# Kernel tuning notes

Hardware: AMD Instinct MI355X
Metric: run time of the kernel (lower is better)

## Reference

```python
import jax, jax.numpy as jnp
import numpy as np

N_NODES = 100000
IN_CH, HIDDEN, OUT_CH = 128, 64, 40
N_EDGES = 1600000


def gcn_conv(x, row, col, W, b, num_nodes):
    """PyG GCNConv: x' = D^-1/2 (A+I) D^-1/2 (x W) + b, self-loops already in row/col."""
    h = x @ W  # [N, out]
    deg = jax.ops.segment_sum(jnp.ones_like(col, dtype=h.dtype), col, num_segments=num_nodes)
    dinv = jnp.where(deg > 0, jax.lax.rsqrt(deg), 0.0)  # [N]
    norm = dinv[row] * dinv[col]  # [E+N]
    msg = h[row] * norm[:, None]  # gather + scale
    out = jax.ops.segment_sum(msg, col, num_segments=num_nodes)  # scatter-add to targets
    return out + b


def setup_inputs() -> dict:
    key = jax.random.key(0)
    k = jax.random.split(key, 6)
    x = jax.random.normal(k[0], (N_NODES, IN_CH), dtype=jnp.float32)
    ei = jax.random.randint(k[1], (2, N_EDGES), 0, N_NODES, dtype=jnp.int64)
    # Glorot-style init for linear weights, zeros for biases (PyG defaults)
    W1 = jax.random.normal(k[2], (IN_CH, HIDDEN), dtype=jnp.float32) / np.sqrt(IN_CH)
    b1 = jnp.zeros((HIDDEN,), dtype=jnp.float32)
    W2 = jax.random.normal(k[3], (HIDDEN, OUT_CH), dtype=jnp.float32) / np.sqrt(HIDDEN)
    b2 = jnp.zeros((OUT_CH,), dtype=jnp.float32)
    return {"x": x, "ei": ei, "W1": W1, "b1": b1, "W2": W2, "b2": b2}


def reference(x, ei, W1, b1, W2, b2):
    num_nodes = x.shape[0]
    loop = jnp.arange(num_nodes, dtype=ei.dtype)
    row = jnp.concatenate([ei[0], loop])  # sources + self-loops
    col = jnp.concatenate([ei[1], loop])  # targets + self-loops
    h = jax.nn.relu(gcn_conv(x, row, col, W1, b1, num_nodes))
    # dropout(p=0.5) is identity in eval mode (deterministic reference)
    return gcn_conv(h, row, col, W2, b2, num_nodes)
```

## Files before the change

kernel.cpp:

```cpp
#include <hip/hip_runtime.h>
#include <hip/hip_bf16.h>
#include <math.h>

#define IN_CH 128
#define HID 64
#define OUT_CH 40
#define NBUCK 1024
#define NBSHIFT 10
#define CAP2 3125
#define CAPL 2560

typedef const __hip_bfloat16* bf16p;
typedef __attribute__((ext_vector_type(8))) short bf16x8;
typedef __attribute__((ext_vector_type(4))) float f32x4;
typedef __attribute__((ext_vector_type(8))) float f32x8;

__device__ __forceinline__ f32x8 cvt8(bf16x8 v) {
    f32x8 o;
    #pragma unroll
    for (int j = 0; j < 8; ++j) {
        unsigned int bits = ((unsigned int)(unsigned short)v[j]) << 16;
        o[j] = __uint_as_float(bits);
    }
    return o;
}

__device__ __forceinline__ bf16x8 pack8(f32x8 v) {
    bf16x8 o;
    #pragma unroll
    for (int j = 0; j < 8; ++j) {
        __hip_bfloat16 b = __float2bfloat16(v[j]);
        o[j] = *reinterpret_cast<short*>(&b);
    }
    return o;
}

__device__ __forceinline__ int bucket_of(int c, int N, float invNB) {
    int b = (int)((float)c * invNB);
    long long cB = (long long)c << NBSHIFT;
    while ((long long)(b + 1) * N <= cB) ++b;
    while (b > 0 && (long long)b * N > cB) --b;
    return b;
}

__global__ __launch_bounds__(256) void k_detectconv(const void* x, const void* ei,
        int* flags, const void* W1, const void* b1, const void* W2, const void* b2,
        float* wf, int* bincnt2) {
    __shared__ int s_f32, s_hi;
    if (threadIdx.x == 0) { s_f32 = 0; s_hi = 0; }
    __syncthreads();
    const __hip_bfloat16* xb = (const __hip_bfloat16*)x;
    const int* ii = (const int*)ei;
    int lf = 0, lh = 0;
    for (int i = threadIdx.x; i < 4096; i += 256) {
        float f = __bfloat162float(xb[i]);
        if (!(fabsf(f) <= 1e4f)) lf = 1;
        lh |= ii[2 * i + 1];
    }
    if (lf) atomicOr(&s_f32, 1);
    if (lh) atomicOr(&s_hi, 1);
    for (int i = threadIdx.x; i < NBUCK; i += 256) bincnt2[i] = 0;
    __syncthreads();
    const int isF32 = s_f32 ? 1 : 0;
    if (threadIdx.x == 0) {
        flags[0] = isF32;
        flags[1] = (s_hi == 0) ? 1 : 0;
        flags[2] = 0;
    }
    for (int i = threadIdx.x; i < 10856; i += 256) {
        const void* src; int off;
        if (i < 8192)       { src = W1; off = i; }
        else if (i < 8256)  { src = b1; off = i - 8192; }
        else if (i < 10816) { src = W2; off = i - 8256; }
        else                { src = b2; off = i - 10816; }
        wf[i] = isF32 ? ((const float*)src)[off]
                      : __bfloat162float(((bf16p)src)[off]);
    }
}

__global__ __launch_bounds__(512) void k_bin2(const int* ei, const int* flags,
        int* bincnt2, unsigned int* bins2, int E, int N, float invNB) {
    __shared__ int cnt[NBUCK], base[NBUCK];
    for (int i = threadIdx.x; i < NBUCK; i += 512) cnt[i] = 0;
    __syncthreads();
    const int i64 = flags[1];
    const int e0 = blockIdx.x * 4096;
    const int e1 = min(e0 + 4096, E);
    int e = e0 + threadIdx.x;
    for (; e + 3 * 512 < e1; e += 4 * 512) {
        int c0 = i64 ? ei[2 * (E + e)]        : ei[E + e];
        int c1 = i64 ? ei[2 * (E + e + 512)]  : ei[E + e + 512];
        int c2 = i64 ? ei[2 * (E + e + 1024)] : ei[E + e + 1024];
        int c3 = i64 ? ei[2 * (E + e + 1536)] : ei[E + e + 1536];
        atomicAdd(&cnt[bucket_of(c0, N, invNB)], 1);
        atomicAdd(&cnt[bucket_of(c1, N, invNB)], 1);
        atomicAdd(&cnt[bucket_of(c2, N, invNB)], 1);
        atomicAdd(&cnt[bucket_of(c3, N, invNB)], 1);
    }
    for (; e < e1; e += 512) {
        int c = i64 ? ei[2 * (E + e)] : ei[E + e];
        atomicAdd(&cnt[bucket_of(c, N, invNB)], 1);
    }
    __syncthreads();
    for (int i = threadIdx.x; i < NBUCK; i += 512) {
        int v = cnt[i];
        base[i] = v ? atomicAdd(&bincnt2[i], v) : 0;
        cnt[i] = 0;
    }
    __syncthreads();
    for (e = e0 + threadIdx.x; e < e1; e += 512) {
        int r, c;
        if (i64) { r = ei[2 * e]; c = ei[2 * (E + e)]; }
        else     { r = ei[e];     c = ei[E + e]; }
        int b = bucket_of(c, N, invNB);
        int nlo = (int)(((long long)b * N + NBUCK - 1) >> NBSHIFT);
        int slot = base[b] + atomicAdd(&cnt[b], 1);
        if (slot < CAP2)
            bins2[(size_t)b * CAP2 + slot] =
                ((unsigned int)r << 7) | (unsigned int)(c - nlo);
    }
}

__global__ __launch_bounds__(256) void k_csr(const unsigned int* bins2, const int* bincnt2,
        int* rowstart, float* dinv, int* erow, int N) {
    __shared__ unsigned int rc[CAPL];
    __shared__ int sdeg[256], lcur[256], red[256];
    const int s = blockIdx.x;
    const int tid = threadIdx.x;
    int part = 0;
    for (int j = tid; j < s; j += 256) part += min(bincnt2[j], CAPL);
    red[tid] = part;
    __syncthreads();
    for (int o = 128; o > 0; o >>= 1) {
        if (tid < o) red[tid] += red[tid + o];
        __syncthreads();
    }
    const int gb = red[0];
    const int nlo = (int)(((long long)s * N + NBUCK - 1) >> NBSHIFT);
    const int nhi = (int)(((long long)(s + 1) * N + NBUCK - 1) >> NBSHIFT);
    const int width = nhi - nlo;
    const int cnt = min(bincnt2[s], CAPL);

    for (int i = tid; i < cnt; i += 256) rc[i] = bins2[(size_t)s * CAP2 + i];
    sdeg[tid] = 0;
    __syncthreads();
    for (int i = tid; i < cnt; i += 256) {
        int j = (int)(rc[i] & 127u);
        if (j < width) atomicAdd(&sdeg[j], 1);
    }
    __syncthreads();
    int my = sdeg[tid];
    __syncthreads();
    for (int off = 1; off < 256; off <<= 1) {
        int t = (tid >= off) ? sdeg[tid - off] : 0;
        __syncthreads();
        sdeg[tid] += t;
        __syncthreads();
    }
    int excl = sdeg[tid] - my;
    lcur[tid] = excl;
    if (tid < width) {
        rowstart[nlo + tid] = gb + excl;
        dinv[nlo + tid] = rsqrtf((float)my + 1.0f);
    }
    if (s == NBUCK - 1 && tid == 0) rowstart[N] = gb + cnt;
    __syncthreads();
    for (int i = tid; i < cnt; i += 256) {
        unsigned int v = rc[i];
        int j = (int)(v & 127u);
        if (j < width) {
            int pos = atomicAdd(&lcur[j], 1);
            erow[gb + pos] = (int)(v >> 7);
        }
    }
}

__global__ __launch_bounds__(256) void k_gemm1_mfma(const void* x, const float* W1f,
        const float* dinv, __hip_bfloat16* h1s, const int* flags, int N) {
    __shared__ __align__(16) unsigned short wT[HID][IN_CH];
    for (int i = threadIdx.x; i < IN_CH * HID; i += 256) {
        int k = i >> 6, c = i & 63;
        __hip_bfloat16 b = __float2bfloat16(W1f[i]);
        wT[c][k] = *reinterpret_cast<unsigned short*>(&b);
    }
    __syncthreads();

    const int isF32 = flags[0];
    const int lane = threadIdx.x & 63;
    const int wid  = threadIdx.x >> 6;
    const int r = lane & 15;
    const int g = lane >> 4;

    bf16x8 bfr[4][4];
    #pragma unroll
    for (int nt = 0; nt < 4; ++nt)
        #pragma unroll
        for (int ks = 0; ks < 4; ++ks)
            bfr[nt][ks] = *(const bf16x8*)&wT[nt * 16 + r][ks * 32 + g * 8];

    const int tiles = (N + 15) >> 4;
    for (int t = blockIdx.x * 4 + wid; t < tiles; t += gridDim.x * 4) {
        const int row0 = t * 16;
        int arow = row0 + r; if (arow >= N) arow = N - 1;
        bf16x8 afr[4];
        if (!isF32) {
            const unsigned short* xr = (const unsigned short*)x + (size_t)arow * IN_CH;
            #pragma unroll
            for (int ks = 0; ks < 4; ++ks)
                afr[ks] = *(const bf16x8*)&xr[ks * 32 + g * 8];
        } else {
            const float* xr = (const float*)x + (size_t)arow * IN_CH;
            #pragma unroll
            for (int ks = 0; ks < 4; ++ks) {
                f32x4 a0 = *(const f32x4*)&xr[ks * 32 + g * 8];
                f32x4 a1 = *(const f32x4*)&xr[ks * 32 + g * 8 + 4];
                #pragma unroll
                for (int j = 0; j < 4; ++j) {
                    __hip_bfloat16 b0 = __float2bfloat16(a0[j]);
                    __hip_bfloat16 b1v = __float2bfloat16(a1[j]);
                    afr[ks][j]     = *reinterpret_cast<short*>(&b0);
                    afr[ks][j + 4] = *reinterpret_cast<short*>(&b1v);
                }
            }
        }
        f32x4 acc[4] = {};
        #pragma unroll
        for (int ks = 0; ks < 4; ++ks)
            #pragma unroll
            for (int nt = 0; nt < 4; ++nt)
                acc[nt] = __builtin_amdgcn_mfma_f32_16x16x32_bf16(afr[ks], bfr[nt][ks],
                                                                  acc[nt], 0, 0, 0);
        #pragma unroll
        for (int q = 0; q < 4; ++q) {
            int rr = row0 + g * 4 + q;
            if (rr < N) {
                float dv = dinv[rr];
                #pragma unroll
                for (int nt = 0; nt < 4; ++nt)
                    h1s[(size_t)rr * HID + nt * 16 + r] =
                        __float2bfloat16(acc[nt][q] * dv);
            }
        }
    }
}

__global__ __launch_bounds__(256) void k_agg1(const int* rowstart, const int* erow,
        const __hip_bfloat16* h1s, const float* dinv, const float* b1f,
        __hip_bfloat16* gs, int N) {
    const int lane = threadIdx.x & 63;
    const int sub = lane >> 3;
    const int co  = lane & 7;
    const f32x4 b1a = *(const f32x4*)&b1f[co * 8];
    const f32x4 b1b = *(const f32x4*)&b1f[co * 8 + 4];
    const int wstride = (gridDim.x * 256) >> 6;
    for (int w = (blockIdx.x * 256 + threadIdx.x) >> 6; w < N; w += wstride) {
        int s0 = __builtin_amdgcn_readfirstlane(rowstart[w]);
        int s1 = __builtin_amdgcn_readfirstlane(rowstart[w + 1]);
        float d = dinv[w];
        bf16x8 sv = *(const bf16x8*)&h1s[(size_t)w * HID + co * 8];
        f32x8 acc = {};
        int i = s0 + sub;
        for (; i + 8 < s1; i += 16) {
            int r0 = erow[i], r1 = erow[i + 8];
            f32x8 v0 = cvt8(*(const bf16x8*)&h1s[(size_t)r0 * HID + co * 8]);
            f32x8 v1 = cvt8(*(const bf16x8*)&h1s[(size_t)r1 * HID + co * 8]);
            #pragma unroll
            for (int j = 0; j < 8; ++j) acc[j] += v0[j] + v1[j];
        }
        if (i < s1) {
            int r0 = erow[i];
            f32x8 v0 = cvt8(*(const bf16x8*)&h1s[(size_t)r0 * HID + co * 8]);
            #pragma unroll
            for (int j = 0; j < 8; ++j) acc[j] += v0[j];
        }
        #pragma unroll
        for (int j = 0; j < 8; ++j) {
            acc[j] += __shfl_xor(acc[j], 8);
            acc[j] += __shfl_xor(acc[j], 16);
            acc[j] += __shfl_xor(acc[j], 32);
        }
        if (sub == 0) {
            f32x8 sf = cvt8(sv);
            f32x8 gv;
            #pragma unroll
            for (int j = 0; j < 4; ++j) {
                float ga = fmaxf(fmaf(d, sf[j] + acc[j], b1a[j]), 0.f);
                float gb = fmaxf(fmaf(d, sf[j + 4] + acc[j + 4], b1b[j]), 0.f);
                gv[j]     = ga * d;
                gv[j + 4] = gb * d;
            }
            *(bf16x8*)&gs[(size_t)w * HID + co * 8] = pack8(gv);
        }
    }
}

__global__ __launch_bounds__(256) void k_agg2s(const int* rowstart, const int* erow,
        const __hip_bfloat16* gs, const float* dinv, __hip_bfloat16* sbuf, int N) {
    const int lane = threadIdx.x & 63;
    const int sub = lane >> 3;
    const int co  = lane & 7;
    const int wstride = (gridDim.x * 256) >> 6;
    for (int w = (blockIdx.x * 256 + threadIdx.x) >> 6; w < N; w += wstride) {
        int s0 = __builtin_amdgcn_readfirstlane(rowstart[w]);
        int s1 = __builtin_amdgcn_readfirstlane(rowstart[w + 1]);
        float d = dinv[w];
        bf16x8 sv = *(const bf16x8*)&gs[(size_t)w * HID + co * 8];
        f32x8 acc = {};
        int i = s0 + sub;
        for (; i + 8 < s1; i += 16) {
            int r0 = erow[i], r1 = erow[i + 8];
            f32x8 v0 = cvt8(*(const bf16x8*)&gs[(size_t)r0 * HID + co * 8]);
            f32x8 v1 = cvt8(*(const bf16x8*)&gs[(size_t)r1 * HID + co * 8]);
            #pragma unroll
            for (int j = 0; j < 8; ++j) acc[j] += v0[j] + v1[j];
        }
        if (i < s1) {
            int r0 = erow[i];
            f32x8 v0 = cvt8(*(const bf16x8*)&gs[(size_t)r0 * HID + co * 8]);
            #pragma unroll
            for (int j = 0; j < 8; ++j) acc[j] += v0[j];
        }
        #pragma unroll
        for (int j = 0; j < 8; ++j) {
            acc[j] += __shfl_xor(acc[j], 8);
            acc[j] += __shfl_xor(acc[j], 16);
            acc[j] += __shfl_xor(acc[j], 32);
        }
        if (sub == 0) {
            f32x8 sf = cvt8(sv);
            f32x8 ov;
            #pragma unroll
            for (int j = 0; j < 8; ++j) ov[j] = d * (sf[j] + acc[j]);
            *(bf16x8*)&sbuf[(size_t)w * HID + co * 8] = pack8(ov);
        }
    }
}

__global__ __launch_bounds__(256) void k_gemm2_mfma(const __hip_bfloat16* sbuf,
        const float* W2f, const float* b2f, float* out, int N) {
    __shared__ __align__(16) unsigned short w2T[48][HID];
    for (int i = threadIdx.x; i < 48 * HID; i += 256) {
        int c = i >> 6, k = i & 63;
        float v = (c < OUT_CH) ? W2f[k * OUT_CH + c] : 0.f;
        __hip_bfloat16 b = __float2bfloat16(v);
        w2T[c][k] = *reinterpret_cast<unsigned short*>(&b);
    }
    __syncthreads();

    const int lane = threadIdx.x & 63;
    const int wid  = threadIdx.x >> 6;
    const int r = lane & 15;
    const int gq = lane >> 4;

    bf16x8 bfr[3][2];
    #pragma unroll
    for (int nt = 0; nt < 3; ++nt)
        #pragma unroll
        for (int ks = 0; ks < 2; ++ks)
            bfr[nt][ks] = *(const bf16x8*)&w2T[nt * 16 + r][ks * 32 + gq * 8];
    float b2v[3];
    #pragma unroll
    for (int nt = 0; nt < 3; ++nt)
        b2v[nt] = (nt * 16 + r < OUT_CH) ? b2f[nt * 16 + r] : 0.f;

    const int tiles = (N + 15) >> 4;
    for (int t = blockIdx.x * 4 + wid; t < tiles; t += gridDim.x * 4) {
        const int row0 = t * 16;
        int arow = row0 + r; if (arow >= N) arow = N - 1;
        const unsigned short* sr = (const unsigned short*)sbuf + (size_t)arow * HID;
        bf16x8 afr[2];
        afr[0] = *(const bf16x8*)&sr[gq * 8];
        afr[1] = *(const bf16x8*)&sr[32 + gq * 8];
        f32x4 acc[3] = {};
        #pragma unroll
        for (int ks = 0; ks < 2; ++ks)
            #pragma unroll
            for (int nt = 0; nt < 3; ++nt)
                acc[nt] = __builtin_amdgcn_mfma_f32_16x16x32_bf16(afr[ks], bfr[nt][ks],
                                                                  acc[nt], 0, 0, 0);
        #pragma unroll
        for (int nt = 0; nt < 3; ++nt) {
            int c = nt * 16 + r;
            #pragma unroll
            for (int q = 0; q < 4; ++q) {
                int rr = row0 + gq * 4 + q;
                if (rr < N && c < OUT_CH)
                    out[(size_t)rr * OUT_CH + c] = acc[nt][q] + b2v[nt];
            }
        }
    }
}

extern "C" void kernel_launch(void* const* d_in, const int* in_sizes, int n_in,
                              void* d_out, int out_size, void* d_ws, size_t ws_size,
                              hipStream_t stream) {
    const void* x  = d_in[0];
    const void* ei = d_in[1];
    const void* W1 = d_in[2];
    const void* b1 = d_in[3];
    const void* W2 = d_in[4];
    const void* b2 = d_in[5];
    const int N = in_sizes[0] / IN_CH;
    const int E = in_sizes[1] / 2;
    const int* eii = (const int*)ei;

    float* ws = (float*)d_ws;
    size_t off = 16;
    int*   flags    = (int*)ws;
    int*   bincnt2  = (int*)ws + off;            off += NBUCK;
    float* dinv     = ws + off;                  off += N;
    float* wf       = ws + off;                  off += 10880;
    int*   rowstart = (int*)ws + off;            off += N + 1;
    off = (off + 255) & ~(size_t)255;
    int*   erow     = (int*)ws + off;            off += E;
    off = (off + 255) & ~(size_t)255;
    __hip_bfloat16* h1s = (__hip_bfloat16*)(ws + off);     off += (size_t)N * HID / 2;
    __hip_bfloat16* gsb = (__hip_bfloat16*)(ws + off);     off += (size_t)N * HID / 2;
    __hip_bfloat16* sbuf = h1s;
    unsigned int* bins2 = (unsigned int*)h1s;

    k_detectconv<<<1, 256, 0, stream>>>(x, ei, flags, W1, b1, W2, b2, wf, bincnt2);

    float invNB = (float)NBUCK / (float)N;
    int nbin = (E + 4095) / 4096;
    k_bin2<<<nbin, 512, 0, stream>>>(eii, flags, bincnt2, bins2, E, N, invNB);
    k_csr<<<NBUCK, 256, 0, stream>>>(bins2, bincnt2, rowstart, dinv, erow, N);

    int tiles = (N + 15) / 16;
    int g1 = (tiles + 7) / 8;
    k_gemm1_mfma<<<g1, 256, 0, stream>>>(x, wf, dinv, h1s, flags, N);

    k_agg1<<<4096, 256, 0, stream>>>(rowstart, erow, h1s, dinv, wf + 8192, gsb, N);
    k_agg2s<<<4096, 256, 0, stream>>>(rowstart, erow, gsb, dinv, sbuf, N);
    k_gemm2_mfma<<<g1, 256, 0, stream>>>(sbuf, wf + 8256, wf + 10816, (float*)d_out, N);
}
```

Measured before the change: 261.1 us.

## Reorder layer-2 to transform before aggregating, and use wave-shuffle scan in CSR build

Layer 2 now multiplies by W2 before aggregation, so the edge gather reads 40-wide bf16 rows instead of 64-wide. Bias is added in the aggregation kernel, which writes the fp32 output directly. The CSR kernel's shared-memory Hillis-Steele scan is replaced by a wave shuffle scan plus a per-wave sum. The binning kernel uses smaller edge chunks, giving more blocks. Rounding changes slightly because the transformed features are stored in bf16 before aggregation. Only 5 of 8 lanes per group do work in the 40-wide gather.

```diff
diff --git a/kernel.cpp b/kernel.cpp
--- a/kernel.cpp
+++ b/kernel.cpp
@@ -84,8 +84,8 @@
     for (int i = threadIdx.x; i < NBUCK; i += 512) cnt[i] = 0;
     __syncthreads();
     const int i64 = flags[1];
-    const int e0 = blockIdx.x * 4096;
-    const int e1 = min(e0 + 4096, E);
+    const int e0 = blockIdx.x * 2048;
+    const int e1 = min(e0 + 2048, E);
     int e = e0 + threadIdx.x;
     for (; e + 3 * 512 < e1; e += 4 * 512) {
         int c0 = i64 ? ei[2 * (E + e)]        : ei[E + e];
@@ -124,9 +124,11 @@
 __global__ __launch_bounds__(256) void k_csr(const unsigned int* bins2, const int* bincnt2,
         int* rowstart, float* dinv, int* erow, int N) {
     __shared__ unsigned int rc[CAPL];
-    __shared__ int sdeg[256], lcur[256], red[256];
+    __shared__ int sdeg[256], lcur[256], red[256], wsums[4];
     const int s = blockIdx.x;
     const int tid = threadIdx.x;
+    const int lane = tid & 63;
+    const int wv = tid >> 6;
     int part = 0;
     for (int j = tid; j < s; j += 256) part += min(bincnt2[j], CAPL);
     red[tid] = part;
@@ -150,14 +152,18 @@
     }
     __syncthreads();
     int my = sdeg[tid];
-    __syncthreads();
-    for (int off = 1; off < 256; off <<= 1) {
-        int t = (tid >= off) ? sdeg[tid - off] : 0;
-        __syncthreads();
-        sdeg[tid] += t;
-        __syncthreads();
-    }
-    int excl = sdeg[tid] - my;
+    int v = my;
+    #pragma unroll
+    for (int off = 1; off < 64; off <<= 1) {
+        int t = __shfl_up(v, off, 64);
+        if (lane >= off) v += t;
+    }
+    if (lane == 63) wsums[wv] = v;
+    __syncthreads();
+    int add = 0;
+    #pragma unroll
+    for (int k = 0; k < 4; ++k) if (k < wv) add += wsums[k];
+    int excl = v + add - my;
     lcur[tid] = excl;
     if (tid < width) {
         rowstart[nlo + tid] = gb + excl;
@@ -166,11 +172,11 @@
     if (s == NBUCK - 1 && tid == 0) rowstart[N] = gb + cnt;
     __syncthreads();
     for (int i = tid; i < cnt; i += 256) {
-        unsigned int v = rc[i];
-        int j = (int)(v & 127u);
+        unsigned int vv = rc[i];
+        int j = (int)(vv & 127u);
         if (j < width) {
             int pos = atomicAdd(&lcur[j], 1);
-            erow[gb + pos] = (int)(v >> 7);
+            erow[gb + pos] = (int)(vv >> 7);
         }
     }
 }
@@ -294,50 +300,8 @@
     }
 }
 
-__global__ __launch_bounds__(256) void k_agg2s(const int* rowstart, const int* erow,
-        const __hip_bfloat16* gs, const float* dinv, __hip_bfloat16* sbuf, int N) {
-    const int lane = threadIdx.x & 63;
-    const int sub = lane >> 3;
-    const int co  = lane & 7;
-    const int wstride = (gridDim.x * 256) >> 6;
-    for (int w = (blockIdx.x * 256 + threadIdx.x) >> 6; w < N; w += wstride) {
-        int s0 = __builtin_amdgcn_readfirstlane(rowstart[w]);
-        int s1 = __builtin_amdgcn_readfirstlane(rowstart[w + 1]);
-        float d = dinv[w];
-        bf16x8 sv = *(const bf16x8*)&gs[(size_t)w * HID + co * 8];
-        f32x8 acc = {};
-        int i = s0 + sub;
-        for (; i + 8 < s1; i += 16) {
-            int r0 = erow[i], r1 = erow[i + 8];
-            f32x8 v0 = cvt8(*(const bf16x8*)&gs[(size_t)r0 * HID + co * 8]);
-            f32x8 v1 = cvt8(*(const bf16x8*)&gs[(size_t)r1 * HID + co * 8]);
-            #pragma unroll
-            for (int j = 0; j < 8; ++j) acc[j] += v0[j] + v1[j];
-        }
-        if (i < s1) {
-            int r0 = erow[i];
-            f32x8 v0 = cvt8(*(const bf16x8*)&gs[(size_t)r0 * HID + co * 8]);
-            #pragma unroll
-            for (int j = 0; j < 8; ++j) acc[j] += v0[j];
-        }
-        #pragma unroll
-        for (int j = 0; j < 8; ++j) {
-            acc[j] += __shfl_xor(acc[j], 8);
-            acc[j] += __shfl_xor(acc[j], 16);
-            acc[j] += __shfl_xor(acc[j], 32);
-        }
-        if (sub == 0) {
-            f32x8 sf = cvt8(sv);
-            f32x8 ov;
-            #pragma unroll
-            for (int j = 0; j < 8; ++j) ov[j] = d * (sf[j] + acc[j]);
-            *(bf16x8*)&sbuf[(size_t)w * HID + co * 8] = pack8(ov);
-        }
-    }
-}
-
-__global__ __launch_bounds__(256) void k_gemm2_mfma(const __hip_bfloat16* sbuf,
-        const float* W2f, const float* b2f, float* out, int N) {
+__global__ __launch_bounds__(256) void k_gemm2t(const __hip_bfloat16* gs,
+        const float* W2f, __hip_bfloat16* ts, int N) {
     __shared__ __align__(16) unsigned short w2T[48][HID];
     for (int i = threadIdx.x; i < 48 * HID; i += 256) {
         int c = i >> 6, k = i & 63;
@@ -358,16 +322,12 @@
         #pragma unroll
         for (int ks = 0; ks < 2; ++ks)
             bfr[nt][ks] = *(const bf16x8*)&w2T[nt * 16 + r][ks * 32 + gq * 8];
-    float b2v[3];
-    #pragma unroll
-    for (int nt = 0; nt < 3; ++nt)
-        b2v[nt] = (nt * 16 + r < OUT_CH) ? b2f[nt * 16 + r] : 0.f;
 
     const int tiles = (N + 15) >> 4;
     for (int t = blockIdx.x * 4 + wid; t < tiles; t += gridDim.x * 4) {
         const int row0 = t * 16;
         int arow = row0 + r; if (arow >= N) arow = N - 1;
-        const unsigned short* sr = (const unsigned short*)sbuf + (size_t)arow * HID;
+        const unsigned short* sr = (const unsigned short*)gs + (size_t)arow * HID;
         bf16x8 afr[2];
         afr[0] = *(const bf16x8*)&sr[gq * 8];
         afr[1] = *(const bf16x8*)&sr[32 + gq * 8];
@@ -385,8 +345,65 @@
             for (int q = 0; q < 4; ++q) {
                 int rr = row0 + gq * 4 + q;
                 if (rr < N && c < OUT_CH)
-                    out[(size_t)rr * OUT_CH + c] = acc[nt][q] + b2v[nt];
-            }
+                    ts[(size_t)rr * OUT_CH + c] = __float2bfloat16(acc[nt][q]);
+            }
+        }
+    }
+}
+
+__global__ __launch_bounds__(256) void k_agg2f(const int* rowstart, const int* erow,
+        const __hip_bfloat16* ts, const float* dinv, const float* b2f,
+        float* out, int N) {
+    const int lane = threadIdx.x & 63;
+    const int sub = lane >> 3;
+    const int co  = lane & 7;
+    const bool act = (co < 5);
+    f32x4 b2a = {}, b2b = {};
+    if (act) {
+        b2a = *(const f32x4*)&b2f[co * 8];
+        b2b = *(const f32x4*)&b2f[co * 8 + 4];
+    }
+    const int wstride = (gridDim.x * 256) >> 6;
+    for (int w = (blockIdx.x * 256 + threadIdx.x) >> 6; w < N; w += wstride) {
+        int s0 = __builtin_amdgcn_readfirstlane(rowstart[w]);
+        int s1 = __builtin_amdgcn_readfirstlane(rowstart[w + 1]);
+        float d = dinv[w];
+        bf16x8 sv = {};
+        if (act) sv = *(const bf16x8*)&ts[(size_t)w * OUT_CH + co * 8];
+        f32x8 acc = {};
+        int i = s0 + sub;
+        for (; i + 8 < s1; i += 16) {
+            int r0 = erow[i], r1 = erow[i + 8];
+            if (act) {
+                f32x8 v0 = cvt8(*(const bf16x8*)&ts[(size_t)r0 * OUT_CH + co * 8]);
+                f32x8 v1 = cvt8(*(const bf16x8*)&ts[(size_t)r1 * OUT_CH + co * 8]);
+                #pragma unroll
+                for (int j = 0; j < 8; ++j) acc[j] += v0[j] + v1[j];
+            }
+        }
+        if (i < s1) {
+            int r0 = erow[i];
+            if (act) {
+                f32x8 v0 = cvt8(*(const bf16x8*)&ts[(size_t)r0 * OUT_CH + co * 8]);
+                #pragma unroll
+                for (int j = 0; j < 8; ++j) acc[j] += v0[j];
+            }
+        }
+        #pragma unroll
+        for (int j = 0; j < 8; ++j) {
+            acc[j] += __shfl_xor(acc[j], 8);
+            acc[j] += __shfl_xor(acc[j], 16);
+            acc[j] += __shfl_xor(acc[j], 32);
+        }
+        if (sub == 0 && act) {
+            f32x8 sf = cvt8(sv);
+            f32x8 ov;
+            #pragma unroll
+            for (int j = 0; j < 4; ++j) {
+                ov[j]     = fmaf(d, sf[j] + acc[j], b2a[j]);
+                ov[j + 4] = fmaf(d, sf[j + 4] + acc[j + 4], b2b[j]);
+            }
+            *(f32x8*)&out[(size_t)w * OUT_CH + co * 8] = ov;
         }
     }
 }
@@ -416,13 +433,13 @@
     off = (off + 255) & ~(size_t)255;
     __hip_bfloat16* h1s = (__hip_bfloat16*)(ws + off);     off += (size_t)N * HID / 2;
     __hip_bfloat16* gsb = (__hip_bfloat16*)(ws + off);     off += (size_t)N * HID / 2;
-    __hip_bfloat16* sbuf = h1s;
     unsigned int* bins2 = (unsigned int*)h1s;
+    __hip_bfloat16* ts  = h1s;
 
     k_detectconv<<<1, 256, 0, stream>>>(x, ei, flags, W1, b1, W2, b2, wf, bincnt2);
 
     float invNB = (float)NBUCK / (float)N;
-    int nbin = (E + 4095) / 4096;
+    int nbin = (E + 2047) / 2048;
     k_bin2<<<nbin, 512, 0, stream>>>(eii, flags, bincnt2, bins2, E, N, invNB);
     k_csr<<<NBUCK, 256, 0, stream>>>(bins2, bincnt2, rowstart, dinv, erow, N);
 
@@ -431,6 +448,7 @@
     k_gemm1_mfma<<<g1, 256, 0, stream>>>(x, wf, dinv, h1s, flags, N);
 
     k_agg1<<<4096, 256, 0, stream>>>(rowstart, erow, h1s, dinv, wf + 8192, gsb, N);
-    k_agg2s<<<4096, 256, 0, stream>>>(rowstart, erow, gsb, dinv, sbuf, N);
-    k_gemm2_mfma<<<g1, 256, 0, stream>>>(sbuf, wf + 8256, wf + 10816, (float*)d_out, N);
-}
+    k_gemm2t<<<g1, 256, 0, stream>>>(gsb, wf + 8256, ts, N);
+    k_agg2f<<<4096, 256, 0, stream>>>(rowstart, erow, ts, dinv, wf + 10816,
+                                      (float*)d_out, N);
+}
```

Measured after the change: 275.4 us. 1.06x slower.
